# Kernel tuning notes

Hardware: AMD Instinct MI355X
Metric: run time of the kernel (lower is better)

Reference implementation:

```python
import jax, jax.numpy as jnp
import numpy as np

P = 2          # patch size
DEPTH = 3
NHEAD = 8
DROP_RATIO = 0.15
LN_EPS = 1e-5


def _ln(x, g, b):
    m = jnp.mean(x, axis=-1, keepdims=True)
    v = jnp.mean((x - m) ** 2, axis=-1, keepdims=True)
    return (x - m) * jax.lax.rsqrt(v + LN_EPS) * g + b


def setup_inputs() -> dict:
    key = jax.random.key(0)
    ks = jax.random.split(key, 16)
    B, C, HW, D, L = 4, 3, 96, 256, DEPTH
    N = (HW // P) ** 2
    s = 0.02
    return {
        "x": jax.random.normal(ks[0], (B, C, HW, HW), jnp.float32),
        "patch_w": jax.random.normal(ks[1], (D, C, P, P), jnp.float32) * s,
        "patch_b": jnp.zeros((D,), jnp.float32),
        "pos": jax.random.normal(ks[2], (1, N, D), jnp.float32) * s,
        "imp_w1": jax.random.normal(ks[3], (D, 256), jnp.float32) * s,
        "imp_b1": jnp.zeros((256,), jnp.float32),
        "imp_w2": jax.random.normal(ks[4], (256, 1), jnp.float32) * s,
        "imp_b2": jnp.zeros((1,), jnp.float32),
        "ln1_g": jnp.ones((L, D), jnp.float32),
        "ln1_b": jnp.zeros((L, D), jnp.float32),
        "qkv_w": jax.random.normal(ks[5], (L, D, 3 * D), jnp.float32) * s,
        "qkv_b": jnp.zeros((L, 3 * D), jnp.float32),
        "proj_w": jax.random.normal(ks[6], (L, D, D), jnp.float32) * s,
        "proj_b": jnp.zeros((L, D), jnp.float32),
        "ln2_g": jnp.ones((L, D), jnp.float32),
        "ln2_b": jnp.zeros((L, D), jnp.float32),
        "mlp_w1": jax.random.normal(ks[7], (L, D, 4 * D), jnp.float32) * s,
        "mlp_b1": jnp.zeros((L, 4 * D), jnp.float32),
        "mlp_w2": jax.random.normal(ks[8], (L, 4 * D, D), jnp.float32) * s,
        "mlp_b2": jnp.zeros((L, D), jnp.float32),
        "out_g": jnp.ones((D,), jnp.float32),
        "out_b": jnp.zeros((D,), jnp.float32),
    }


def reference(x, patch_w, patch_b, pos, imp_w1, imp_b1, imp_w2, imp_b2,
              ln1_g, ln1_b, qkv_w, qkv_b, proj_w, proj_b,
              ln2_g, ln2_b, mlp_w1, mlp_b1, mlp_w2, mlp_b2, out_g, out_b):
    B, C, H, W = x.shape
    D = patch_w.shape[0]
    Hc, Wc = H // P, W // P
    # Patch embed: conv(k=stride=P) == blocked einsum  -> (B, N, D)
    xr = x.reshape(B, C, Hc, P, Wc, P)
    tokens = jnp.einsum('bchpwq,dcpq->bhwd', xr, patch_w).reshape(B, Hc * Wc, D) + patch_b
    tokens = tokens + pos
    B, N, _ = tokens.shape

    # Importance scores -> bottom-k keys masked (Eq.8-10)
    h = jax.nn.relu(tokens @ imp_w1 + imp_b1)
    scores = jax.nn.sigmoid((h @ imp_w2 + imp_b2)[..., 0])  # (B, N)
    k = int(DROP_RATIO * N)
    _, idx = jax.lax.top_k(-scores, k)                      # k smallest scores
    md = jnp.zeros((B, N), bool).at[jnp.arange(B)[:, None], idx].set(True)

    dk = D // NHEAD
    scale = 1.0 / np.sqrt(dk)
    for l in range(DEPTH):
        hln = _ln(tokens, ln1_g[l], ln1_b[l])
        qkv = hln @ qkv_w[l] + qkv_b[l]
        q, kk, v = jnp.split(qkv, 3, axis=-1)
        q = q.reshape(B, N, NHEAD, dk).transpose(0, 2, 1, 3)
        kk = kk.reshape(B, N, NHEAD, dk).transpose(0, 2, 1, 3)
        v = v.reshape(B, N, NHEAD, dk).transpose(0, 2, 1, 3)
        logits = jnp.einsum('bhnd,bhmd->bhnm', q, kk) * scale
        logits = jnp.where(md[:, None, None, :], -jnp.inf, logits)
        attn = jax.nn.softmax(logits, axis=-1)
        out = jnp.einsum('bhnm,bhmd->bhnd', attn, v)
        out = out.transpose(0, 2, 1, 3).reshape(B, N, D)
        tokens = tokens + (out @ proj_w[l] + proj_b[l])
        h2 = _ln(tokens, ln2_g[l], ln2_b[l])
        tokens = tokens + (jax.nn.gelu(h2 @ mlp_w1[l] + mlp_b1[l], approximate=False) @ mlp_w2[l] + mlp_b2[l])

    tokens = _ln(tokens, out_g, out_b)
    return tokens.mean(axis=1)  # (B, D)
```

## Files before the change

kernel.cpp:

```cpp
#include <hip/hip_runtime.h>
#include <hip/hip_bf16.h>
#include <math.h>

#define BATCH 4
#define NTOK  2304
#define DIM   256
#define NHEADS 8
#define HCDIM 48
#define KSEL  345
#define NKEEP 1959
#define NKC   1984
#define KT    31
#define KREM  39
#define LN_EPS 1e-5f

typedef unsigned short u16;
typedef __attribute__((ext_vector_type(8))) short bf16x8;
typedef __attribute__((ext_vector_type(4))) float f32x4;

__device__ __forceinline__ u16 f2bf(float x) {
  union { float f; unsigned u; } v; v.f = x;
  return (u16)((v.u + 0x7FFFu + ((v.u >> 16) & 1u)) >> 16);
}

__device__ __forceinline__ void gload_lds16(const u16* g, u16* l) {
  __builtin_amdgcn_global_load_lds((const __attribute__((address_space(1))) void*)g,
                                   (__attribute__((address_space(3))) void*)l, 16, 0, 0);
}

__global__ __launch_bounds__(256) void k_patch_embed(
    const float* __restrict__ x, const float* __restrict__ pw,
    const float* __restrict__ pb, const float* __restrict__ pos,
    float* __restrict__ tokens) {
  int blk = blockIdx.x;
  int b = blk / NTOK, n = blk % NTOK;
  int hc = n / HCDIM, wc = n % HCDIM;
  __shared__ float xs[12];
  int t = threadIdx.x;
  if (t < 12) {
    int c = t >> 2, p = (t >> 1) & 1, q = t & 1;
    xs[t] = x[((b * 3 + c) * 96 + (hc * 2 + p)) * 96 + (wc * 2 + q)];
  }
  __syncthreads();
  float acc = pb[t];
#pragma unroll
  for (int i = 0; i < 12; ++i) acc += xs[i] * pw[t * 12 + i];
  tokens[(size_t)(b * NTOK + n) * DIM + t] = acc + pos[n * DIM + t];
}

__global__ __launch_bounds__(256) void k_importance(
    const float* __restrict__ tokens, const float* __restrict__ w1,
    const float* __restrict__ b1, const float* __restrict__ w2,
    const float* __restrict__ b2, float* __restrict__ scores) {
  __shared__ float ts[16 * 256];
  __shared__ float hw[16 * 256];
  int base = blockIdx.x * 16;
  int t = threadIdx.x;
  for (int i = t; i < 16 * 256; i += 256) ts[i] = tokens[(size_t)base * 256 + i];
  __syncthreads();
  float acc[16];
#pragma unroll
  for (int r = 0; r < 16; ++r) acc[r] = b1[t];
  for (int i = 0; i < 256; ++i) {
    float w = w1[i * 256 + t];
#pragma unroll
    for (int r = 0; r < 16; ++r) acc[r] += ts[r * 256 + i] * w;
  }
  float w2v = w2[t];
#pragma unroll
  for (int r = 0; r < 16; ++r) hw[r * 256 + t] = fmaxf(acc[r], 0.f) * w2v;
  __syncthreads();
  if (t < 16) {
    float s = b2[0];
    for (int i = 0; i < 256; ++i) s += hw[t * 256 + i];
    scores[base + t] = 1.f / (1.f + expf(-s));
  }
}

__global__ __launch_bounds__(256) void k_select(const float* __restrict__ scores,
                                                int* __restrict__ cmap,
                                                u16* __restrict__ kvc) {
  int b = blockIdx.x, t = threadIdx.x;
  __shared__ unsigned sb[NTOK];
  __shared__ int cnt;
  __shared__ int pfl[256], pfe[256];
  __shared__ int remS;
  for (int i = t; i < NTOK; i += 256) sb[i] = __float_as_uint(scores[b * NTOK + i]);
  __syncthreads();
  unsigned prefix = 0;
  int r = KSEL;
  for (int bit = 31; bit >= 0; --bit) {
    if (t == 0) cnt = 0;
    __syncthreads();
    unsigned bmask = 1u << bit;
    unsigned hmask = (bit == 31) ? 0u : ~((bmask << 1) - 1u);
    int local = 0;
    for (int i = t; i < NTOK; i += 256)
      if ((sb[i] & hmask) == prefix && !(sb[i] & bmask)) local++;
    if (local) atomicAdd(&cnt, local);
    __syncthreads();
    int c0 = cnt;
    if (r > c0) { r -= c0; prefix |= bmask; }
    __syncthreads();
  }
  unsigned v = prefix;
  int cl = 0, ce = 0;
  int j0 = t * 9;
  for (int j = j0; j < j0 + 9; ++j) { cl += (sb[j] < v); ce += (sb[j] == v); }
  pfl[t] = cl; pfe[t] = ce;
  __syncthreads();
  if (t == 0) {
    int pl = 0, pe = 0;
    for (int i = 0; i < 256; ++i) {
      int a = pfl[i], e = pfe[i];
      pfl[i] = pl; pfe[i] = pe;
      pl += a; pe += e;
    }
    remS = KSEL - pl;
  }
  __syncthreads();
  int pl = pfl[t], pe = pfe[t], rem = remS;
  for (int j = j0; j < j0 + 9; ++j) {
    bool less = sb[j] < v, eq = sb[j] == v;
    bool drop = less || (eq && pe < rem);
    int dropped_before = pl + (pe < rem ? pe : rem);
    cmap[b * NTOK + j] = drop ? -1 : (j - dropped_before);
    pl += less; pe += eq;
  }
  for (int i = t; i < (NKC - NKEEP) * 512; i += 256)
    kvc[((size_t)b * NKC + NKEEP) * 512 + i] = 0;
}

__global__ __launch_bounds__(256) void k_ln4bf(
    const float* __restrict__ in, u16* __restrict__ out,
    const float* __restrict__ g, const float* __restrict__ bta) {
  int w = threadIdx.x >> 6, l = threadIdx.x & 63;
  size_t row = (size_t)blockIdx.x * 4 + w;
  float4 v = *(const float4*)(in + row * DIM + l * 4);
  float s = v.x + v.y + v.z + v.w;
  float ss = v.x * v.x + v.y * v.y + v.z * v.z + v.w * v.w;
#pragma unroll
  for (int o = 1; o < 64; o <<= 1) { s += __shfl_xor(s, o); ss += __shfl_xor(ss, o); }
  float m = s * (1.f / DIM);
  float inv = rsqrtf(ss * (1.f / DIM) - m * m + LN_EPS);
  float4 gv = *(const float4*)(g + l * 4);
  float4 bv = *(const float4*)(bta + l * 4);
  union { ushort4 u4; __hip_bfloat162 h2[2]; } o4;
  o4.h2[0] = __float22bfloat162_rn(make_float2((v.x - m) * inv * gv.x + bv.x,
                                               (v.y - m) * inv * gv.y + bv.y));
  o4.h2[1] = __float22bfloat162_rn(make_float2((v.z - m) * inv * gv.z + bv.z,
                                               (v.w - m) * inv * gv.w + bv.w));
  *(ushort4*)(out + row * DIM + l * 4) = o4.u4;
}

__global__ __launch_bounds__(256) void k_lnmean(
    const float* __restrict__ in, const float* __restrict__ g,
    const float* __restrict__ bta, float* __restrict__ part) {
  int chunk = blockIdx.x, b = blockIdx.y;
  int w = threadIdx.x >> 6, l = threadIdx.x & 63;
  float4 gv = *(const float4*)(g + l * 4);
  float4 bv = *(const float4*)(bta + l * 4);
  float4 acc = make_float4(0.f, 0.f, 0.f, 0.f);
  for (int i = 0; i < 16; ++i) {
    size_t row = (size_t)b * NTOK + chunk * 64 + w * 16 + i;
    float4 v = *(const float4*)(in + row * DIM + l * 4);
    float s = v.x + v.y + v.z + v.w;
    float ss = v.x * v.x + v.y * v.y + v.z * v.z + v.w * v.w;
#pragma unroll
    for (int o = 1; o < 64; o <<= 1) { s += __shfl_xor(s, o); ss += __shfl_xor(ss, o); }
    float m = s * (1.f / DIM);
    float inv = rsqrtf(ss * (1.f / DIM) - m * m + LN_EPS);
    acc.x += (v.x - m) * inv * gv.x + bv.x;
    acc.y += (v.y - m) * inv * gv.y + bv.y;
    acc.z += (v.z - m) * inv * gv.z + bv.z;
    acc.w += (v.w - m) * inv * gv.w + bv.w;
  }
  __shared__ float4 red[4][64];
  red[w][l] = acc;
  __syncthreads();
  if (w == 0) {
    float4 a0 = red[0][l], a1 = red[1][l], a2 = red[2][l], a3 = red[3][l];
    float4 tot = make_float4(a0.x + a1.x + a2.x + a3.x, a0.y + a1.y + a2.y + a3.y,
                             a0.z + a1.z + a2.z + a3.z, a0.w + a1.w + a2.w + a3.w);
    *(float4*)(part + ((size_t)b * 36 + chunk) * DIM + l * 4) = tot;
  }
}

__global__ __launch_bounds__(256) void k_mean_final(const float* __restrict__ part,
                                                    float* __restrict__ out) {
  int b = blockIdx.x, d = threadIdx.x;
  float s = 0.f;
  for (int c = 0; c < 36; ++c) s += part[(size_t)(b * 36 + c) * DIM + d];
  out[b * DIM + d] = s * (1.0f / NTOK);
}

__global__ __launch_bounds__(256) void k_wtrans(const float* __restrict__ W,
                                               u16* __restrict__ WT, int K, int N) {
  __shared__ float tile[32][33];
  int nb = blockIdx.x * 32, kb = blockIdx.y * 32;
  const float* Wl = W + (size_t)blockIdx.z * K * N;
  u16* WTl = WT + (size_t)blockIdx.z * K * N;
  int tx = threadIdx.x & 31, ty = threadIdx.x >> 5;
  for (int i = 0; i < 32; i += 8) tile[ty + i][tx] = Wl[(size_t)(kb + ty + i) * N + nb + tx];
  __syncthreads();
  for (int i = 0; i < 32; i += 8)
    WTl[(size_t)(nb + ty + i) * K + kb + tx] = f2bf(tile[tx][ty + i]);
}

__global__ __launch_bounds__(256) void k_gemm_bf16(
    const u16* __restrict__ A, const u16* __restrict__ BT,
    const float* __restrict__ bias, u16* __restrict__ outb,
    int K, int N, int act) {
  __shared__ __align__(16) u16 As[128 * 32];
  __shared__ __align__(16) u16 Bs[128 * 32];
  int t = threadIdx.x;
  int m0 = blockIdx.y * 128, n0 = blockIdx.x * 128;
  int w = t >> 6, l = t & 63, lr = l & 15, qd = l >> 4;
  int wm = (w >> 1) * 64, wn = (w & 1) * 64;
  const u16* gA = A + (size_t)(m0 + w * 16 + (l >> 2)) * K + (l & 3) * 8;
  const u16* gA2 = gA + (size_t)64 * K;
  const u16* gB = BT + (size_t)(n0 + w * 16 + (l >> 2)) * K + (l & 3) * 8;
  const u16* gB2 = gB + (size_t)64 * K;
  f32x4 acc[4][4];
#pragma unroll
  for (int i = 0; i < 4; ++i)
#pragma unroll
    for (int j = 0; j < 4; ++j)
#pragma unroll
      for (int r = 0; r < 4; ++r) acc[i][j][r] = 0.f;
  for (int k0 = 0; k0 < K; k0 += 32) {
    gload_lds16(gA + k0, As + w * 512);
    gload_lds16(gA2 + k0, As + 2048 + w * 512);
    gload_lds16(gB + k0, Bs + w * 512);
    gload_lds16(gB2 + k0, Bs + 2048 + w * 512);
    __syncthreads();
    bf16x8 af[4], bfr[4];
#pragma unroll
    for (int mt = 0; mt < 4; ++mt)
      af[mt] = *(const bf16x8*)(As + (wm + mt * 16 + lr) * 32 + qd * 8);
#pragma unroll
    for (int nt = 0; nt < 4; ++nt)
      bfr[nt] = *(const bf16x8*)(Bs + (wn + nt * 16 + lr) * 32 + qd * 8);
#pragma unroll
    for (int mt = 0; mt < 4; ++mt)
#pragma unroll
      for (int nt = 0; nt < 4; ++nt)
        acc[mt][nt] = __builtin_amdgcn_mfma_f32_16x16x32_bf16(af[mt], bfr[nt],
                                                              acc[mt][nt], 0, 0, 0);
    __syncthreads();
  }
#pragma unroll
  for (int mt = 0; mt < 4; ++mt) {
#pragma unroll
    for (int nt = 0; nt < 4; ++nt) {
#pragma unroll
      for (int r = 0; r < 4; ++r) {
        size_t m = (size_t)m0 + wm + mt * 16 + qd * 4 + r;
        int c = n0 + wn + nt * 16 + lr;
        float val = acc[mt][nt][r] + bias[c];
        if (act) val = 0.5f * val * (1.f + erff(val * 0.70710678118654752f));
        outb[m * N + c] = f2bf(val);
      }
    }
  }
}

__global__ __launch_bounds__(256) void k_gemm_qkv(
    const u16* __restrict__ A, const u16* __restrict__ BT,
    const float* __restrict__ bias, const int* __restrict__ cmap,
    u16* __restrict__ Qb, u16* __restrict__ KVc) {
  const int K = 256, N = 768;
  __shared__ __align__(16) u16 As[128 * 32];
  __shared__ __align__(16) u16 Bs[128 * 32];
  int t = threadIdx.x;
  int m0 = blockIdx.y * 128, n0 = blockIdx.x * 128;
  int w = t >> 6, l = t & 63, lr = l & 15, qd = l >> 4;
  int wm = (w >> 1) * 64, wn = (w & 1) * 64;
  const u16* gA = A + (size_t)(m0 + w * 16 + (l >> 2)) * K + (l & 3) * 8;
  const u16* gA2 = gA + (size_t)64 * K;
  const u16* gB = BT + (size_t)(n0 + w * 16 + (l >> 2)) * K + (l & 3) * 8;
  const u16* gB2 = gB + (size_t)64 * K;
  f32x4 acc[4][4];
#pragma unroll
  for (int i = 0; i < 4; ++i)
#pragma unroll
    for (int j = 0; j < 4; ++j)
#pragma unroll
      for (int r = 0; r < 4; ++r) acc[i][j][r] = 0.f;
  for (int k0 = 0; k0 < K; k0 += 32) {
    gload_lds16(gA + k0, As + w * 512);
    gload_lds16(gA2 + k0, As + 2048 + w * 512);
    gload_lds16(gB + k0, Bs + w * 512);
    gload_lds16(gB2 + k0, Bs + 2048 + w * 512);
    __syncthreads();
    bf16x8 af[4], bfr[4];
#pragma unroll
    for (int mt = 0; mt < 4; ++mt)
      af[mt] = *(const bf16x8*)(As + (wm + mt * 16 + lr) * 32 + qd * 8);
#pragma unroll
    for (int nt = 0; nt < 4; ++nt)
      bfr[nt] = *(const bf16x8*)(Bs + (wn + nt * 16 + lr) * 32 + qd * 8);
#pragma unroll
    for (int mt = 0; mt < 4; ++mt)
#pragma unroll
      for (int nt = 0; nt < 4; ++nt)
        acc[mt][nt] = __builtin_amdgcn_mfma_f32_16x16x32_bf16(af[mt], bfr[nt],
                                                              acc[mt][nt], 0, 0, 0);
    __syncthreads();
  }
  bool isQ = (n0 + wn) < 256;
#pragma unroll
  for (int mt = 0; mt < 4; ++mt) {
#pragma unroll
    for (int r = 0; r < 4; ++r) {
      int m = m0 + wm + mt * 16 + qd * 4 + r;
      int cpos = isQ ? 0 : cmap[m];
      int b = m / NTOK;
#pragma unroll
      for (int nt = 0; nt < 4; ++nt) {
        int c = n0 + wn + nt * 16 + lr;
        float val = acc[mt][nt][r] + bias[c];
        if (isQ) {
          Qb[(size_t)m * 256 + c] = f2bf(val * 0.17677669529663687f);
        } else if (cpos >= 0) {
          KVc[((size_t)b * NKC + cpos) * 512 + (c - 256)] = f2bf(val);
        }
      }
    }
  }
}

__global__ __launch_bounds__(256) void k_gemm_n64(
    const u16* __restrict__ A, const u16* __restrict__ BT,
    const float* __restrict__ bias, const float* __restrict__ res,
    float* __restrict__ outf, int K, int N) {
  __shared__ __align__(16) u16 As[128 * 32];
  __shared__ __align__(16) u16 Bs[64 * 32];
  int t = threadIdx.x;
  int m0 = blockIdx.y * 128, n0 = blockIdx.x * 64;
  int w = t >> 6, l = t & 63, lr = l & 15, qd = l >> 4;
  int wm = (w >> 1) * 64, wn = (w & 1) * 32;
  const u16* gA = A + (size_t)(m0 + w * 16 + (l >> 2)) * K + (l & 3) * 8;
  const u16* gA2 = gA + (size_t)64 * K;
  const u16* gB = BT + (size_t)(n0 + w * 16 + (l >> 2)) * K + (l & 3) * 8;
  f32x4 acc[4][2];
#pragma unroll
  for (int i = 0; i < 4; ++i)
#pragma unroll
    for (int j = 0; j < 2; ++j)
#pragma unroll
      for (int r = 0; r < 4; ++r) acc[i][j][r] = 0.f;
  for (int k0 = 0; k0 < K; k0 += 32) {
    gload_lds16(gA + k0, As + w * 512);
    gload_lds16(gA2 + k0, As + 2048 + w * 512);
    gload_lds16(gB + k0, Bs + w * 512);
    __syncthreads();
    bf16x8 af[4], bfr[2];
#pragma unroll
    for (int mt = 0; mt < 4; ++mt)
      af[mt] = *(const bf16x8*)(As + (wm + mt * 16 + lr) * 32 + qd * 8);
#pragma unroll
    for (int nt = 0; nt < 2; ++nt)
      bfr[nt] = *(const bf16x8*)(Bs + (wn + nt * 16 + lr) * 32 + qd * 8);
#pragma unroll
    for (int mt = 0; mt < 4; ++mt)
#pragma unroll
      for (int nt = 0; nt < 2; ++nt)
        acc[mt][nt] = __builtin_amdgcn_mfma_f32_16x16x32_bf16(af[mt], bfr[nt],
                                                              acc[mt][nt], 0, 0, 0);
    __syncthreads();
  }
#pragma unroll
  for (int mt = 0; mt < 4; ++mt) {
#pragma unroll
    for (int nt = 0; nt < 2; ++nt) {
#pragma unroll
      for (int r = 0; r < 4; ++r) {
        size_t m = (size_t)m0 + wm + mt * 16 + qd * 4 + r;
        int c = n0 + wn + nt * 16 + lr;
        outf[m * N + c] = acc[mt][nt][r] + bias[c] + res[m * N + c];
      }
    }
  }
}

__global__ __launch_bounds__(256) void k_attn3(
    const u16* __restrict__ Qb, const u16* __restrict__ KVc,
    u16* __restrict__ outb) {
  int qt = blockIdx.x, h = blockIdx.y, b = blockIdx.z;
  int t = threadIdx.x, w = t >> 6, l = t & 63, lr = l & 15, qd = l >> 4;
  __shared__ __align__(16) u16 Ks[2][64 * 32];
  __shared__ __align__(16) u16 Vt[2][32][72];
  __shared__ __align__(16) u16 Pq[4][16][72];
  __shared__ float ls[4][16];
  int q0 = qt * 64 + w * 16;
  bf16x8 qf = *(const bf16x8*)(Qb + ((size_t)(b * NTOK) + q0 + lr) * 256 + h * 32 + qd * 8);
  const u16* kvb = KVc + (size_t)b * NKC * 512;
  const u16* gK = kvb + (size_t)(t >> 2) * 512 + h * 32 + (t & 3) * 8;
  const u16* gV = kvb + (size_t)l * 512 + 256 + h * 32 + w * 8;
  gload_lds16(gK, &Ks[0][w * 512]);
  bf16x8 vr = *(const bf16x8*)(gV);
  f32x4 oa[2];
  float l_run = 0.f;
#pragma unroll
  for (int r = 0; r < 4; ++r) { oa[0][r] = 0.f; oa[1][r] = 0.f; }
  for (int kt = 0; kt < KT; ++kt) {
    int buf = kt & 1;
#pragma unroll
    for (int j = 0; j < 8; ++j) Vt[buf][w * 8 + j][l] = (u16)vr[j];
    __syncthreads();
    if (kt + 1 < KT) {
      size_t off = (size_t)(kt + 1) * 64 * 512;
      gload_lds16(gK + off, &Ks[buf ^ 1][w * 512]);
      vr = *(const bf16x8*)(gV + off);
    }
    f32x4 p4[4];
#pragma unroll
    for (int nt = 0; nt < 4; ++nt) {
      bf16x8 kf = *(const bf16x8*)(&Ks[buf][(nt * 16 + lr) * 32 + qd * 8]);
      f32x4 z; z[0] = 0.f; z[1] = 0.f; z[2] = 0.f; z[3] = 0.f;
      p4[nt] = __builtin_amdgcn_mfma_f32_16x16x32_bf16(kf, qf, z, 0, 0, 0);
    }
#pragma unroll
    for (int nt = 0; nt < 4; ++nt)
#pragma unroll
      for (int r = 0; r < 4; ++r) p4[nt][r] = __expf(p4[nt][r]);
    if (kt == KT - 1) {
#pragma unroll
      for (int nt = 0; nt < 4; ++nt)
#pragma unroll
        for (int r = 0; r < 4; ++r)
          p4[nt][r] = (nt * 16 + qd * 4 + r < KREM) ? p4[nt][r] : 0.f;
    }
    float psum = 0.f;
#pragma unroll
    for (int nt = 0; nt < 4; ++nt)
#pragma unroll
      for (int r = 0; r < 4; ++r) psum += p4[nt][r];
    psum += __shfl_xor(psum, 16);
    psum += __shfl_xor(psum, 32);
    l_run += psum;
#pragma unroll
    for (int nt = 0; nt < 4; ++nt) {
      union { ushort4 u4; __hip_bfloat162 h2[2]; } pu;
      pu.h2[0] = __float22bfloat162_rn(make_float2(p4[nt][0], p4[nt][1]));
      pu.h2[1] = __float22bfloat162_rn(make_float2(p4[nt][2], p4[nt][3]));
      *(ushort4*)(&Pq[w][lr][nt * 16 + qd * 4]) = pu.u4;
    }
#pragma unroll
    for (int kh = 0; kh < 2; ++kh) {
      bf16x8 pf = *(const bf16x8*)(&Pq[w][lr][kh * 32 + qd * 8]);
#pragma unroll
      for (int dh = 0; dh < 2; ++dh) {
        bf16x8 vf = *(const bf16x8*)(&Vt[buf][dh * 16 + lr][kh * 32 + qd * 8]);
        oa[dh] = __builtin_amdgcn_mfma_f32_16x16x32_bf16(pf, vf, oa[dh], 0, 0, 0);
      }
    }
  }
  if (qd == 0) ls[w][lr] = l_run;
#pragma unroll
  for (int r = 0; r < 4; ++r) {
    float inv = 1.f / ls[w][qd * 4 + r];
    size_t row = (size_t)b * NTOK + q0 + qd * 4 + r;
    outb[row * 256 + h * 32 + lr] = f2bf(oa[0][r] * inv);
    outb[row * 256 + h * 32 + 16 + lr] = f2bf(oa[1][r] * inv);
  }
}

extern "C" void kernel_launch(void* const* d_in, const int* in_sizes, int n_in,
                              void* d_out, int out_size, void* d_ws, size_t ws_size,
                              hipStream_t stream) {
  (void)in_sizes; (void)n_in; (void)out_size;
  const float* x       = (const float*)d_in[0];
  const float* patch_w = (const float*)d_in[1];
  const float* patch_b = (const float*)d_in[2];
  const float* pos     = (const float*)d_in[3];
  const float* imp_w1  = (const float*)d_in[4];
  const float* imp_b1  = (const float*)d_in[5];
  const float* imp_w2  = (const float*)d_in[6];
  const float* imp_b2  = (const float*)d_in[7];
  const float* ln1_g   = (const float*)d_in[8];
  const float* ln1_b   = (const float*)d_in[9];
  const float* qkv_w   = (const float*)d_in[10];
  const float* qkv_b   = (const float*)d_in[11];
  const float* proj_w  = (const float*)d_in[12];
  const float* proj_b  = (const float*)d_in[13];
  const float* ln2_g   = (const float*)d_in[14];
  const float* ln2_b   = (const float*)d_in[15];
  const float* mlp_w1  = (const float*)d_in[16];
  const float* mlp_b1  = (const float*)d_in[17];
  const float* mlp_w2  = (const float*)d_in[18];
  const float* mlp_b2  = (const float*)d_in[19];
  const float* out_g   = (const float*)d_in[20];
  const float* out_b   = (const float*)d_in[21];
  float* out = (float*)d_out;

  const int M = BATCH * NTOK;
  const size_t TOK = (size_t)M * DIM;

  char* p = (char*)d_ws;
  float* tokens = (float*)p;       p += TOK * 4;
  float* scoresp = (float*)p;      p += (size_t)M * 4;
  int* cmap = (int*)p;             p += (size_t)M * 4;
  u16* act_bf = (u16*)p;           p += TOK * 2;
  u16* Qb = (u16*)p;               p += TOK * 2;
  u16* kvc = (u16*)p;              p += (size_t)BATCH * NKC * 512 * 2;
  u16* big_bf = (u16*)p;           p += (size_t)M * 1024 * 2;
  u16* wq_t = (u16*)p;             p += (size_t)3 * 768 * 256 * 2;
  u16* wp_t = (u16*)p;             p += (size_t)3 * 256 * 256 * 2;
  u16* w1_t = (u16*)p;             p += (size_t)3 * 1024 * 256 * 2;
  u16* w2_t = (u16*)p;             p += (size_t)3 * 256 * 1024 * 2;
  float* partials = (float*)act_bf;
  if (ws_size < (size_t)(p - (char*)d_ws)) return;

  k_wtrans<<<dim3(768 / 32, 256 / 32, 3), 256, 0, stream>>>(qkv_w, wq_t, 256, 768);
  k_wtrans<<<dim3(256 / 32, 256 / 32, 3), 256, 0, stream>>>(proj_w, wp_t, 256, 256);
  k_wtrans<<<dim3(1024 / 32, 256 / 32, 3), 256, 0, stream>>>(mlp_w1, w1_t, 256, 1024);
  k_wtrans<<<dim3(256 / 32, 1024 / 32, 3), 256, 0, stream>>>(mlp_w2, w2_t, 1024, 256);

  k_patch_embed<<<dim3(M), 256, 0, stream>>>(x, patch_w, patch_b, pos, tokens);
  k_importance<<<dim3(M / 16), 256, 0, stream>>>(tokens, imp_w1, imp_b1, imp_w2, imp_b2, scoresp);
  k_select<<<dim3(BATCH), 256, 0, stream>>>(scoresp, cmap, kvc);

  for (int l = 0; l < 3; ++l) {
    k_ln4bf<<<dim3(M / 4), 256, 0, stream>>>(tokens, act_bf, ln1_g + l * DIM, ln1_b + l * DIM);
    k_gemm_qkv<<<dim3(6, 72), 256, 0, stream>>>(
        act_bf, wq_t + (size_t)l * 768 * 256, qkv_b + l * 768, cmap, Qb, kvc);
    k_attn3<<<dim3(36, NHEADS, BATCH), 256, 0, stream>>>(Qb, kvc, act_bf);
    k_gemm_n64<<<dim3(4, 72), 256, 0, stream>>>(
        act_bf, wp_t + (size_t)l * 256 * 256, proj_b + l * DIM, tokens, tokens, 256, 256);
    k_ln4bf<<<dim3(M / 4), 256, 0, stream>>>(tokens, act_bf, ln2_g + l * DIM, ln2_b + l * DIM);
    k_gemm_bf16<<<dim3(8, 72), 256, 0, stream>>>(
        act_bf, w1_t + (size_t)l * 1024 * 256, mlp_b1 + l * 1024, big_bf, 256, 1024, 1);
    k_gemm_n64<<<dim3(4, 72), 256, 0, stream>>>(
        big_bf, w2_t + (size_t)l * 256 * 1024, mlp_b2 + l * DIM, tokens, tokens, 1024, 256);
  }
  k_lnmean<<<dim3(36, BATCH), 256, 0, stream>>>(tokens, out_g, out_b, partials);
  k_mean_final<<<dim3(BATCH), 256, 0, stream>>>(partials, out);
}
```

Measured before the change: 605.6 us.

## Double-buffer GEMM LDS tiles, widen attention query tile, fuse weight transposes

The three GEMM kernels now double-buffer their A/B LDS tiles, prefetching the next K chunk while MFMAs run on the current one, which removes one barrier per iteration. The attention kernel gives each wave 32 queries instead of 16, so every K/V tile loaded is reused across twice as many queries and the grid is halved. It also computes the softmax row sums with an MFMA against a ones vector instead of shuffle reductions. The four weight-transpose launches are merged into one. In exchange LDS use and register pressure go up, which may lower occupancy.

```diff
diff --git a/kernel.cpp b/kernel.cpp
--- a/kernel.cpp
+++ b/kernel.cpp
@@ -194,12 +194,23 @@
   out[b * DIM + d] = s * (1.0f / NTOK);
 }
 
-__global__ __launch_bounds__(256) void k_wtrans(const float* __restrict__ W,
-                                               u16* __restrict__ WT, int K, int N) {
+__global__ __launch_bounds__(256) void k_wtrans_all(
+    const float* __restrict__ qkv_w, const float* __restrict__ proj_w,
+    const float* __restrict__ mlp_w1, const float* __restrict__ mlp_w2,
+    u16* __restrict__ wq, u16* __restrict__ wp,
+    u16* __restrict__ w1, u16* __restrict__ w2) {
+  int id = blockIdx.x;
+  const float* W; u16* WT; int K, N, m;
+  if (id < 576)       { m = id;        K = 256;  N = 768;  W = qkv_w;  WT = wq; }
+  else if (id < 768)  { m = id - 576;  K = 256;  N = 256;  W = proj_w; WT = wp; }
+  else if (id < 1536) { m = id - 768;  K = 256;  N = 1024; W = mlp_w1; WT = w1; }
+  else                { m = id - 1536; K = 1024; N = 256;  W = mlp_w2; WT = w2; }
+  int ntiles = N / 32, tilesPerLayer = ntiles * (K / 32);
+  int layer = m / tilesPerLayer, tid = m % tilesPerLayer;
+  int nb = (tid % ntiles) * 32, kb = (tid / ntiles) * 32;
+  const float* Wl = W + (size_t)layer * K * N;
+  u16* WTl = WT + (size_t)layer * K * N;
   __shared__ float tile[32][33];
-  int nb = blockIdx.x * 32, kb = blockIdx.y * 32;
-  const float* Wl = W + (size_t)blockIdx.z * K * N;
-  u16* WTl = WT + (size_t)blockIdx.z * K * N;
   int tx = threadIdx.x & 31, ty = threadIdx.x >> 5;
   for (int i = 0; i < 32; i += 8) tile[ty + i][tx] = Wl[(size_t)(kb + ty + i) * N + nb + tx];
   __syncthreads();
@@ -211,8 +222,8 @@
     const u16* __restrict__ A, const u16* __restrict__ BT,
     const float* __restrict__ bias, u16* __restrict__ outb,
     int K, int N, int act) {
-  __shared__ __align__(16) u16 As[128 * 32];
-  __shared__ __align__(16) u16 Bs[128 * 32];
+  __shared__ __align__(16) u16 As[2][128 * 32];
+  __shared__ __align__(16) u16 Bs[2][128 * 32];
   int t = threadIdx.x;
   int m0 = blockIdx.y * 128, n0 = blockIdx.x * 128;
   int w = t >> 6, l = t & 63, lr = l & 15, qd = l >> 4;
@@ -228,26 +239,34 @@
     for (int j = 0; j < 4; ++j)
 #pragma unroll
       for (int r = 0; r < 4; ++r) acc[i][j][r] = 0.f;
-  for (int k0 = 0; k0 < K; k0 += 32) {
-    gload_lds16(gA + k0, As + w * 512);
-    gload_lds16(gA2 + k0, As + 2048 + w * 512);
-    gload_lds16(gB + k0, Bs + w * 512);
-    gload_lds16(gB2 + k0, Bs + 2048 + w * 512);
-    __syncthreads();
+  gload_lds16(gA, As[0] + w * 512);
+  gload_lds16(gA2, As[0] + 2048 + w * 512);
+  gload_lds16(gB, Bs[0] + w * 512);
+  gload_lds16(gB2, Bs[0] + 2048 + w * 512);
+  int nchunks = K >> 5;
+  for (int c = 0; c < nchunks; ++c) {
+    int buf = c & 1;
+    __syncthreads();
+    if (c + 1 < nchunks) {
+      int k0 = (c + 1) << 5;
+      gload_lds16(gA + k0, As[buf ^ 1] + w * 512);
+      gload_lds16(gA2 + k0, As[buf ^ 1] + 2048 + w * 512);
+      gload_lds16(gB + k0, Bs[buf ^ 1] + w * 512);
+      gload_lds16(gB2 + k0, Bs[buf ^ 1] + 2048 + w * 512);
+    }
     bf16x8 af[4], bfr[4];
 #pragma unroll
     for (int mt = 0; mt < 4; ++mt)
-      af[mt] = *(const bf16x8*)(As + (wm + mt * 16 + lr) * 32 + qd * 8);
+      af[mt] = *(const bf16x8*)(As[buf] + (wm + mt * 16 + lr) * 32 + qd * 8);
 #pragma unroll
     for (int nt = 0; nt < 4; ++nt)
-      bfr[nt] = *(const bf16x8*)(Bs + (wn + nt * 16 + lr) * 32 + qd * 8);
+      bfr[nt] = *(const bf16x8*)(Bs[buf] + (wn + nt * 16 + lr) * 32 + qd * 8);
 #pragma unroll
     for (int mt = 0; mt < 4; ++mt)
 #pragma unroll
       for (int nt = 0; nt < 4; ++nt)
         acc[mt][nt] = __builtin_amdgcn_mfma_f32_16x16x32_bf16(af[mt], bfr[nt],
                                                               acc[mt][nt], 0, 0, 0);
-    __syncthreads();
   }
 #pragma unroll
   for (int mt = 0; mt < 4; ++mt) {
@@ -270,8 +289,8 @@
     const float* __restrict__ bias, const int* __restrict__ cmap,
     u16* __restrict__ Qb, u16* __restrict__ KVc) {
   const int K = 256, N = 768;
-  __shared__ __align__(16) u16 As[128 * 32];
-  __shared__ __align__(16) u16 Bs[128 * 32];
+  __shared__ __align__(16) u16 As[2][128 * 32];
+  __shared__ __align__(16) u16 Bs[2][128 * 32];
   int t = threadIdx.x;
   int m0 = blockIdx.y * 128, n0 = blockIdx.x * 128;
   int w = t >> 6, l = t & 63, lr = l & 15, qd = l >> 4;
@@ -287,26 +306,33 @@
     for (int j = 0; j < 4; ++j)
 #pragma unroll
       for (int r = 0; r < 4; ++r) acc[i][j][r] = 0.f;
-  for (int k0 = 0; k0 < K; k0 += 32) {
-    gload_lds16(gA + k0, As + w * 512);
-    gload_lds16(gA2 + k0, As + 2048 + w * 512);
-    gload_lds16(gB + k0, Bs + w * 512);
-    gload_lds16(gB2 + k0, Bs + 2048 + w * 512);
-    __syncthreads();
+  gload_lds16(gA, As[0] + w * 512);
+  gload_lds16(gA2, As[0] + 2048 + w * 512);
+  gload_lds16(gB, Bs[0] + w * 512);
+  gload_lds16(gB2, Bs[0] + 2048 + w * 512);
+  for (int c = 0; c < 8; ++c) {
+    int buf = c & 1;
+    __syncthreads();
+    if (c + 1 < 8) {
+      int k0 = (c + 1) << 5;
+      gload_lds16(gA + k0, As[buf ^ 1] + w * 512);
+      gload_lds16(gA2 + k0, As[buf ^ 1] + 2048 + w * 512);
+      gload_lds16(gB + k0, Bs[buf ^ 1] + w * 512);
+      gload_lds16(gB2 + k0, Bs[buf ^ 1] + 2048 + w * 512);
+    }
     bf16x8 af[4], bfr[4];
 #pragma unroll
     for (int mt = 0; mt < 4; ++mt)
-      af[mt] = *(const bf16x8*)(As + (wm + mt * 16 + lr) * 32 + qd * 8);
+      af[mt] = *(const bf16x8*)(As[buf] + (wm + mt * 16 + lr) * 32 + qd * 8);
 #pragma unroll
     for (int nt = 0; nt < 4; ++nt)
-      bfr[nt] = *(const bf16x8*)(Bs + (wn + nt * 16 + lr) * 32 + qd * 8);
+      bfr[nt] = *(const bf16x8*)(Bs[buf] + (wn + nt * 16 + lr) * 32 + qd * 8);
 #pragma unroll
     for (int mt = 0; mt < 4; ++mt)
 #pragma unroll
       for (int nt = 0; nt < 4; ++nt)
         acc[mt][nt] = __builtin_amdgcn_mfma_f32_16x16x32_bf16(af[mt], bfr[nt],
                                                               acc[mt][nt], 0, 0, 0);
-    __syncthreads();
   }
   bool isQ = (n0 + wn) < 256;
 #pragma unroll
@@ -334,8 +360,8 @@
     const u16* __restrict__ A, const u16* __restrict__ BT,
     const float* __restrict__ bias, const float* __restrict__ res,
     float* __restrict__ outf, int K, int N) {
-  __shared__ __align__(16) u16 As[128 * 32];
-  __shared__ __align__(16) u16 Bs[64 * 32];
+  __shared__ __align__(16) u16 As[2][128 * 32];
+  __shared__ __align__(16) u16 Bs[2][64 * 32];
   int t = threadIdx.x;
   int m0 = blockIdx.y * 128, n0 = blockIdx.x * 64;
   int w = t >> 6, l = t & 63, lr = l & 15, qd = l >> 4;
@@ -350,25 +376,32 @@
     for (int j = 0; j < 2; ++j)
 #pragma unroll
       for (int r = 0; r < 4; ++r) acc[i][j][r] = 0.f;
-  for (int k0 = 0; k0 < K; k0 += 32) {
-    gload_lds16(gA + k0, As + w * 512);
-    gload_lds16(gA2 + k0, As + 2048 + w * 512);
-    gload_lds16(gB + k0, Bs + w * 512);
-    __syncthreads();
+  gload_lds16(gA, As[0] + w * 512);
+  gload_lds16(gA2, As[0] + 2048 + w * 512);
+  gload_lds16(gB, Bs[0] + w * 512);
+  int nchunks = K >> 5;
+  for (int c = 0; c < nchunks; ++c) {
+    int buf = c & 1;
+    __syncthreads();
+    if (c + 1 < nchunks) {
+      int k0 = (c + 1) << 5;
+      gload_lds16(gA + k0, As[buf ^ 1] + w * 512);
+      gload_lds16(gA2 + k0, As[buf ^ 1] + 2048 + w * 512);
+      gload_lds16(gB + k0, Bs[buf ^ 1] + w * 512);
+    }
     bf16x8 af[4], bfr[2];
 #pragma unroll
     for (int mt = 0; mt < 4; ++mt)
-      af[mt] = *(const bf16x8*)(As + (wm + mt * 16 + lr) * 32 + qd * 8);
+      af[mt] = *(const bf16x8*)(As[buf] + (wm + mt * 16 + lr) * 32 + qd * 8);
 #pragma unroll
     for (int nt = 0; nt < 2; ++nt)
-      bfr[nt] = *(const bf16x8*)(Bs + (wn + nt * 16 + lr) * 32 + qd * 8);
+      bfr[nt] = *(const bf16x8*)(Bs[buf] + (wn + nt * 16 + lr) * 32 + qd * 8);
 #pragma unroll
     for (int mt = 0; mt < 4; ++mt)
 #pragma unroll
       for (int nt = 0; nt < 2; ++nt)
         acc[mt][nt] = __builtin_amdgcn_mfma_f32_16x16x32_bf16(af[mt], bfr[nt],
                                                               acc[mt][nt], 0, 0, 0);
-    __syncthreads();
   }
 #pragma unroll
   for (int mt = 0; mt < 4; ++mt) {
@@ -384,26 +417,34 @@
   }
 }
 
-__global__ __launch_bounds__(256) void k_attn3(
+__global__ __launch_bounds__(256) void k_attn4(
     const u16* __restrict__ Qb, const u16* __restrict__ KVc,
     u16* __restrict__ outb) {
   int qt = blockIdx.x, h = blockIdx.y, b = blockIdx.z;
   int t = threadIdx.x, w = t >> 6, l = t & 63, lr = l & 15, qd = l >> 4;
   __shared__ __align__(16) u16 Ks[2][64 * 32];
-  __shared__ __align__(16) u16 Vt[2][32][72];
-  __shared__ __align__(16) u16 Pq[4][16][72];
-  __shared__ float ls[4][16];
-  int q0 = qt * 64 + w * 16;
-  bf16x8 qf = *(const bf16x8*)(Qb + ((size_t)(b * NTOK) + q0 + lr) * 256 + h * 32 + qd * 8);
+  __shared__ __align__(16) u16 Vt[2][32][80];
+  __shared__ __align__(16) u16 Pq[4][32][80];
+  const short ONE = (short)0x3F80;
+  int q0 = qt * 128 + w * 32;
   const u16* kvb = KVc + (size_t)b * NKC * 512;
+  bf16x8 qf[2];
+  qf[0] = *(const bf16x8*)(Qb + ((size_t)(b * NTOK) + q0 + lr) * 256 + h * 32 + qd * 8);
+  qf[1] = *(const bf16x8*)(Qb + ((size_t)(b * NTOK) + q0 + 16 + lr) * 256 + h * 32 + qd * 8);
   const u16* gK = kvb + (size_t)(t >> 2) * 512 + h * 32 + (t & 3) * 8;
   const u16* gV = kvb + (size_t)l * 512 + 256 + h * 32 + w * 8;
   gload_lds16(gK, &Ks[0][w * 512]);
   bf16x8 vr = *(const bf16x8*)(gV);
-  f32x4 oa[2];
-  float l_run = 0.f;
-#pragma unroll
-  for (int r = 0; r < 4; ++r) { oa[0][r] = 0.f; oa[1][r] = 0.f; }
+  f32x4 oa[2][2];
+  f32x4 lacc[2];
+#pragma unroll
+  for (int r = 0; r < 4; ++r) {
+    oa[0][0][r] = 0.f; oa[0][1][r] = 0.f; oa[1][0][r] = 0.f; oa[1][1][r] = 0.f;
+    lacc[0][r] = 0.f; lacc[1][r] = 0.f;
+  }
+  bf16x8 ones;
+#pragma unroll
+  for (int j = 0; j < 8; ++j) ones[j] = ONE;
   for (int kt = 0; kt < KT; ++kt) {
     int buf = kt & 1;
 #pragma unroll
@@ -414,56 +455,59 @@
       gload_lds16(gK + off, &Ks[buf ^ 1][w * 512]);
       vr = *(const bf16x8*)(gV + off);
     }
-    f32x4 p4[4];
-#pragma unroll
-    for (int nt = 0; nt < 4; ++nt) {
-      bf16x8 kf = *(const bf16x8*)(&Ks[buf][(nt * 16 + lr) * 32 + qd * 8]);
-      f32x4 z; z[0] = 0.f; z[1] = 0.f; z[2] = 0.f; z[3] = 0.f;
-      p4[nt] = __builtin_amdgcn_mfma_f32_16x16x32_bf16(kf, qf, z, 0, 0, 0);
-    }
+    bf16x8 kf[4];
 #pragma unroll
     for (int nt = 0; nt < 4; ++nt)
-#pragma unroll
-      for (int r = 0; r < 4; ++r) p4[nt][r] = __expf(p4[nt][r]);
+      kf[nt] = *(const bf16x8*)(&Ks[buf][(nt * 16 + lr) * 32 + qd * 8]);
+#pragma unroll
+    for (int qh = 0; qh < 2; ++qh) {
+      f32x4 p4[4];
+#pragma unroll
+      for (int nt = 0; nt < 4; ++nt) {
+        f32x4 z; z[0] = 0.f; z[1] = 0.f; z[2] = 0.f; z[3] = 0.f;
+        p4[nt] = __builtin_amdgcn_mfma_f32_16x16x32_bf16(kf[nt], qf[qh], z, 0, 0, 0);
+      }
+#pragma unroll
+      for (int nt = 0; nt < 4; ++nt)
+#pragma unroll
+        for (int r = 0; r < 4; ++r) p4[nt][r] = __expf(p4[nt][r]);
+#pragma unroll
+      for (int nt = 0; nt < 4; ++nt) {
+        union { ushort4 u4; __hip_bfloat162 h2[2]; } pu;
+        pu.h2[0] = __float22bfloat162_rn(make_float2(p4[nt][0], p4[nt][1]));
+        pu.h2[1] = __float22bfloat162_rn(make_float2(p4[nt][2], p4[nt][3]));
+        *(ushort4*)(&Pq[w][qh * 16 + lr][nt * 16 + qd * 4]) = pu.u4;
+      }
+    }
+    bf16x8 of1 = ones;
     if (kt == KT - 1) {
 #pragma unroll
-      for (int nt = 0; nt < 4; ++nt)
-#pragma unroll
-        for (int r = 0; r < 4; ++r)
-          p4[nt][r] = (nt * 16 + qd * 4 + r < KREM) ? p4[nt][r] : 0.f;
-    }
-    float psum = 0.f;
-#pragma unroll
-    for (int nt = 0; nt < 4; ++nt)
-#pragma unroll
-      for (int r = 0; r < 4; ++r) psum += p4[nt][r];
-    psum += __shfl_xor(psum, 16);
-    psum += __shfl_xor(psum, 32);
-    l_run += psum;
-#pragma unroll
-    for (int nt = 0; nt < 4; ++nt) {
-      union { ushort4 u4; __hip_bfloat162 h2[2]; } pu;
-      pu.h2[0] = __float22bfloat162_rn(make_float2(p4[nt][0], p4[nt][1]));
-      pu.h2[1] = __float22bfloat162_rn(make_float2(p4[nt][2], p4[nt][3]));
-      *(ushort4*)(&Pq[w][lr][nt * 16 + qd * 4]) = pu.u4;
-    }
-#pragma unroll
-    for (int kh = 0; kh < 2; ++kh) {
-      bf16x8 pf = *(const bf16x8*)(&Pq[w][lr][kh * 32 + qd * 8]);
-#pragma unroll
-      for (int dh = 0; dh < 2; ++dh) {
-        bf16x8 vf = *(const bf16x8*)(&Vt[buf][dh * 16 + lr][kh * 32 + qd * 8]);
-        oa[dh] = __builtin_amdgcn_mfma_f32_16x16x32_bf16(pf, vf, oa[dh], 0, 0, 0);
+      for (int j = 0; j < 8; ++j) of1[j] = (32 + qd * 8 + j < KREM) ? ONE : (short)0;
+    }
+#pragma unroll
+    for (int qh = 0; qh < 2; ++qh) {
+#pragma unroll
+      for (int kh = 0; kh < 2; ++kh) {
+        bf16x8 pf = *(const bf16x8*)(&Pq[w][qh * 16 + lr][kh * 32 + qd * 8]);
+#pragma unroll
+        for (int dh = 0; dh < 2; ++dh) {
+          bf16x8 vf = *(const bf16x8*)(&Vt[buf][dh * 16 + lr][kh * 32 + qd * 8]);
+          oa[qh][dh] = __builtin_amdgcn_mfma_f32_16x16x32_bf16(pf, vf, oa[qh][dh], 0, 0, 0);
+        }
+        lacc[qh] = __builtin_amdgcn_mfma_f32_16x16x32_bf16(
+            pf, kh ? of1 : ones, lacc[qh], 0, 0, 0);
       }
     }
   }
-  if (qd == 0) ls[w][lr] = l_run;
-#pragma unroll
-  for (int r = 0; r < 4; ++r) {
-    float inv = 1.f / ls[w][qd * 4 + r];
-    size_t row = (size_t)b * NTOK + q0 + qd * 4 + r;
-    outb[row * 256 + h * 32 + lr] = f2bf(oa[0][r] * inv);
-    outb[row * 256 + h * 32 + 16 + lr] = f2bf(oa[1][r] * inv);
+#pragma unroll
+  for (int qh = 0; qh < 2; ++qh) {
+#pragma unroll
+    for (int r = 0; r < 4; ++r) {
+      float inv = 1.f / lacc[qh][r];
+      size_t row = (size_t)b * NTOK + q0 + qh * 16 + qd * 4 + r;
+      outb[row * 256 + h * 32 + lr] = f2bf(oa[qh][0][r] * inv);
+      outb[row * 256 + h * 32 + 16 + lr] = f2bf(oa[qh][1][r] * inv);
+    }
   }
 }
 
@@ -513,11 +557,8 @@
   float* partials = (float*)act_bf;
   if (ws_size < (size_t)(p - (char*)d_ws)) return;
 
-  k_wtrans<<<dim3(768 / 32, 256 / 32, 3), 256, 0, stream>>>(qkv_w, wq_t, 256, 768);
-  k_wtrans<<<dim3(256 / 32, 256 / 32, 3), 256, 0, stream>>>(proj_w, wp_t, 256, 256);
-  k_wtrans<<<dim3(1024 / 32, 256 / 32, 3), 256, 0, stream>>>(mlp_w1, w1_t, 256, 1024);
-  k_wtrans<<<dim3(256 / 32, 1024 / 32, 3), 256, 0, stream>>>(mlp_w2, w2_t, 1024, 256);
-
+  k_wtrans_all<<<dim3(2304), 256, 0, stream>>>(qkv_w, proj_w, mlp_w1, mlp_w2,
+                                               wq_t, wp_t, w1_t, w2_t);
   k_patch_embed<<<dim3(M), 256, 0, stream>>>(x, patch_w, patch_b, pos, tokens);
   k_importance<<<dim3(M / 16), 256, 0, stream>>>(tokens, imp_w1, imp_b1, imp_w2, imp_b2, scoresp);
   k_select<<<dim3(BATCH), 256, 0, stream>>>(scoresp, cmap, kvc);
@@ -526,7 +567,7 @@
     k_ln4bf<<<dim3(M / 4), 256, 0, stream>>>(tokens, act_bf, ln1_g + l * DIM, ln1_b + l * DIM);
     k_gemm_qkv<<<dim3(6, 72), 256, 0, stream>>>(
         act_bf, wq_t + (size_t)l * 768 * 256, qkv_b + l * 768, cmap, Qb, kvc);
-    k_attn3<<<dim3(36, NHEADS, BATCH), 256, 0, stream>>>(Qb, kvc, act_bf);
+    k_attn4<<<dim3(18, NHEADS, BATCH), 256, 0, stream>>>(Qb, kvc, act_bf);
     k_gemm_n64<<<dim3(4, 72), 256, 0, stream>>>(
         act_bf, wp_t + (size_t)l * 256 * 256, proj_b + l * DIM, tokens, tokens, 256, 256);
     k_ln4bf<<<dim3(M / 4), 256, 0, stream>>>(tokens, act_bf, ln2_g + l * DIM, ln2_b + l * DIM);
```

Result: no change. 613.6 us (+1.3%).
